# Kernel optimization log

Hardware: AMD Instinct MI355X
Metric: run time of the kernel (lower is better)

Reference implementation:

```python
import jax, jax.numpy as jnp
import numpy as np

D_MODEL = 1024
NUM_HEADS = 16
D_K = D_MODEL // NUM_HEADS
SCALE = float(np.sqrt(D_K))


def setup_inputs() -> dict:
    key = jax.random.key(0)
    ks = jax.random.split(key, 11)
    B, S = 4, 2048
    std = 1.0 / np.sqrt(D_MODEL)
    return {
        "query": jax.random.normal(ks[0], (B, S, D_MODEL), jnp.float32),
        "key": jax.random.normal(ks[1], (B, S, D_MODEL), jnp.float32),
        "value": jax.random.normal(ks[2], (B, S, D_MODEL), jnp.float32),
        "w_q": jax.random.normal(ks[3], (D_MODEL, D_MODEL), jnp.float32) * std,
        "b_q": jnp.zeros((D_MODEL,), jnp.float32),
        "w_k": jax.random.normal(ks[4], (D_MODEL, D_MODEL), jnp.float32) * std,
        "b_k": jnp.zeros((D_MODEL,), jnp.float32),
        "w_v": jax.random.normal(ks[5], (D_MODEL, D_MODEL), jnp.float32) * std,
        "b_v": jnp.zeros((D_MODEL,), jnp.float32),
        "w_o": jax.random.normal(ks[6], (D_MODEL, D_MODEL), jnp.float32) * std,
        "b_o": jnp.zeros((D_MODEL,), jnp.float32),
    }


def reference(query, key, value, w_q, b_q, w_k, b_k, w_v, b_v, w_o, b_o):
    B, S, _ = query.shape
    # torch Linear: x @ W.T + b
    def proj(x, w, b):
        y = x @ w.T + b                      # [B,S,D]
        return y.reshape(B, -1, NUM_HEADS, D_K).transpose(0, 2, 1, 3)  # [B,H,S,dk]

    Q = proj(query, w_q, b_q)
    K = proj(key, w_k, b_k)
    V = proj(value, w_v, b_v)

    scores = jnp.einsum("bhqd,bhkd->bhqk", Q, K) / SCALE   # [B,H,S,S]
    attn = jax.nn.softmax(scores, axis=-1)                  # dropout = identity (eval)
    ctx = jnp.einsum("bhqk,bhkd->bhqd", attn, V)            # [B,H,S,dk]
    ctx = ctx.transpose(0, 2, 1, 3).reshape(B, -1, D_MODEL) # [B,S,D]
    out = ctx @ w_o.T + b_o
    return out, attn
```

## Files before the change

kernel.cpp:

```cpp
#include <hip/hip_runtime.h>

typedef __bf16 bf16;
typedef __bf16 bf16x8 __attribute__((ext_vector_type(8)));
typedef __bf16 bf16x4 __attribute__((ext_vector_type(4)));
typedef float f32x4 __attribute__((ext_vector_type(4)));

#define B_SZ   4
#define S_LEN  2048
#define DM     1024
#define NH     16
#define DKH    64
#define MROWS  (B_SZ * S_LEN)

#if __has_builtin(__builtin_amdgcn_exp2f)
#define EXP2(x) __builtin_amdgcn_exp2f(x)
#else
#define EXP2(x) exp2f(x)
#endif

__device__ __forceinline__ int swz_(int row) { return ((row ^ (row >> 3)) & 7) << 4; }

__device__ __forceinline__ void gload_lds16(const void* g, void* l) {
  __builtin_amdgcn_global_load_lds(
      (const __attribute__((address_space(1))) void*)g,
      (__attribute__((address_space(3))) void*)l, 16, 0, 0);
}

__global__ __launch_bounds__(256) void cvt_f32_bf16(const float* __restrict__ in,
                                                    bf16* __restrict__ out, int n8) {
  for (int i = blockIdx.x * blockDim.x + threadIdx.x; i < n8; i += gridDim.x * blockDim.x) {
    const float4* p = (const float4*)(in + (size_t)i * 8);
    float4 a = p[0], b = p[1];
    bf16x8 o;
    o[0] = (bf16)a.x; o[1] = (bf16)a.y; o[2] = (bf16)a.z; o[3] = (bf16)a.w;
    o[4] = (bf16)b.x; o[5] = (bf16)b.y; o[6] = (bf16)b.z; o[7] = (bf16)b.w;
    *(bf16x8*)(out + (size_t)i * 8) = o;
  }
}

template <int MODE>
__global__ __launch_bounds__(256) void gemm_bt(const bf16* __restrict__ A,
                                               const bf16* __restrict__ Bm,
                                               const float* __restrict__ bias,
                                               void* __restrict__ out) {
  constexpr int BM = 128, BN = 128, BK = 64, K = DM, N = DM;
  __shared__ bf16 As[BM * BK];
  __shared__ bf16 Bs[BN * BK];
  const int tid = threadIdx.x;
  const int l = tid & 63;
  const int w = tid >> 6;
  const int wr = w >> 1, wc = w & 1;
  const int m0 = (blockIdx.x >> 3) * BM;
  const int n0 = (blockIdx.x & 7) * BN;
  const int lrow = l & 15;
  const int lk = (l >> 4) * 8;

  f32x4 acc[4][4] = {};

  for (int kt = 0; kt < K; kt += BK) {
    __syncthreads();
#pragma unroll
    for (int r = 0; r < 4; ++r) {
      int c = r * 256 + tid;
      int row = c >> 3;
      int cb = ((c & 7) * 16) ^ swz_(row);
      gload_lds16((const char*)(A + (size_t)(m0 + row) * K + kt) + cb, (char*)As + c * 16);
      gload_lds16((const char*)(Bm + (size_t)(n0 + row) * K + kt) + cb, (char*)Bs + c * 16);
    }
    __syncthreads();
#pragma unroll
    for (int kk = 0; kk < BK; kk += 32) {
      bf16x8 a[4], b[4];
#pragma unroll
      for (int i = 0; i < 4; ++i) {
        int ar = wr * 64 + i * 16 + lrow;
        int br = wc * 64 + i * 16 + lrow;
        a[i] = *(const bf16x8*)((const char*)As + ar * 128 + (((kk + lk) * 2) ^ swz_(ar)));
        b[i] = *(const bf16x8*)((const char*)Bs + br * 128 + (((kk + lk) * 2) ^ swz_(br)));
      }
#pragma unroll
      for (int i = 0; i < 4; ++i)
#pragma unroll
        for (int j = 0; j < 4; ++j)
          acc[i][j] = __builtin_amdgcn_mfma_f32_16x16x32_bf16(a[i], b[j], acc[i][j], 0, 0, 0);
    }
  }

#pragma unroll
  for (int i = 0; i < 4; ++i) {
#pragma unroll
    for (int j = 0; j < 4; ++j) {
#pragma unroll
      for (int r = 0; r < 4; ++r) {
        int row = m0 + wr * 64 + i * 16 + (l >> 4) * 4 + r;
        int col = n0 + wc * 64 + j * 16 + (l & 15);
        float v = acc[i][j][r] + bias[col];
        if (MODE == 0) {
          int bb = row >> 11, ss = row & 2047, hh = col >> 6, dd = col & 63;
          ((bf16*)out)[(((size_t)bb * NH + hh) * S_LEN + ss) * DKH + dd] = (bf16)v;
        } else {
          ((float*)out)[(size_t)row * N + col] = v;
        }
      }
    }
  }
}

__global__ __launch_bounds__(256, 3) void attn_fused(const bf16* __restrict__ Q,
                                                     const bf16* __restrict__ Kg,
                                                     const bf16* __restrict__ Vg,
                                                     float* __restrict__ attn,
                                                     bf16* __restrict__ ctx) {
  constexpr int QT = 128, KT = 64, PSP = 72, NT = S_LEN / KT;
  __shared__ bf16 Ks[KT * DKH];
  __shared__ bf16 Vts[DKH * KT];
  __shared__ bf16 Ps[QT * PSP];

  const int tid = threadIdx.x, l = tid & 63, w = tid >> 6;
  const int bh = blockIdx.x >> 4;
  const int q0 = (blockIdx.x & 15) * QT;
  const bf16* Qb = Q + (size_t)bh * S_LEN * DKH;
  const bf16* Kb = Kg + (size_t)bh * S_LEN * DKH;
  const bf16* Vb = Vg + (size_t)bh * S_LEN * DKH;
  const int lrow = l & 15, lk = (l >> 4) * 8;
  const int g4 = (l >> 4) * 4;
  const float c2 = 0.18033688011f;

  bf16x8 qf[2][2];
#pragma unroll
  for (int m = 0; m < 2; ++m)
#pragma unroll
    for (int h = 0; h < 2; ++h)
      qf[m][h] = *(const bf16x8*)(Qb + (size_t)(q0 + w * 32 + m * 16 + lrow) * DKH + h * 32 + lk);

  auto stageK = [&](int kt) {
#pragma unroll
    for (int r = 0; r < 2; ++r) {
      int c = r * 256 + tid;
      int row = c >> 3;
      int cb = ((c & 7) * 16) ^ swz_(row);
      gload_lds16((const char*)(Kb + (size_t)(kt + row) * DKH) + cb, (char*)Ks + c * 16);
    }
  };

  float lsum[2] = {0.f, 0.f};
  for (int t = 0; t < NT; ++t) {
    __syncthreads();
    stageK(t * KT);
    __syncthreads();
    f32x4 st[2][4] = {};
#pragma unroll
    for (int h = 0; h < 2; ++h)
#pragma unroll
      for (int n = 0; n < 4; ++n) {
        int kr = n * 16 + lrow;
        bf16x8 b = *(const bf16x8*)((const char*)Ks + kr * 128 + (((h * 32 + lk) * 2) ^ swz_(kr)));
        st[0][n] = __builtin_amdgcn_mfma_f32_16x16x32_bf16(b, qf[0][h], st[0][n], 0, 0, 0);
        st[1][n] = __builtin_amdgcn_mfma_f32_16x16x32_bf16(b, qf[1][h], st[1][n], 0, 0, 0);
      }
#pragma unroll
    for (int m = 0; m < 2; ++m)
#pragma unroll
      for (int n = 0; n < 4; ++n)
#pragma unroll
        for (int r = 0; r < 4; ++r)
          lsum[m] += EXP2(st[m][n][r] * c2);
  }

  float invl[2];
#pragma unroll
  for (int m = 0; m < 2; ++m) {
    float ll = lsum[m];
    ll += __shfl_xor(ll, 16);
    ll += __shfl_xor(ll, 32);
    invl[m] = 1.0f / ll;
  }

  f32x4 oc[2][4] = {};
  for (int t = 0; t < NT; ++t) {
    const int kt = t * KT;
    __syncthreads();
    stageK(kt);
    bf16x8 vv[2];
#pragma unroll
    for (int r = 0; r < 2; ++r) {
      int c = r * 256 + tid;
      vv[r] = *(const bf16x8*)(Vb + (size_t)(kt + (c >> 3)) * DKH + (c & 7) * 8);
    }
#pragma unroll
    for (int r = 0; r < 2; ++r) {
      int c = r * 256 + tid;
      int kv = c >> 3, d0 = (c & 7) * 8;
#pragma unroll
      for (int j = 0; j < 8; ++j) {
        int row = d0 + j;
        *(bf16*)((char*)Vts + row * 128 + ((kv * 2) ^ swz_(row))) = vv[r][j];
      }
    }
    __syncthreads();
    f32x4 st[2][4] = {};
#pragma unroll
    for (int h = 0; h < 2; ++h)
#pragma unroll
      for (int n = 0; n < 4; ++n) {
        int kr = n * 16 + lrow;
        bf16x8 b = *(const bf16x8*)((const char*)Ks + kr * 128 + (((h * 32 + lk) * 2) ^ swz_(kr)));
        st[0][n] = __builtin_amdgcn_mfma_f32_16x16x32_bf16(b, qf[0][h], st[0][n], 0, 0, 0);
        st[1][n] = __builtin_amdgcn_mfma_f32_16x16x32_bf16(b, qf[1][h], st[1][n], 0, 0, 0);
      }
#pragma unroll
    for (int m = 0; m < 2; ++m) {
      const int qr = w * 32 + m * 16 + lrow;
      float* arow = attn + (size_t)bh * S_LEN * S_LEN + (size_t)(q0 + qr) * S_LEN + kt + g4;
#pragma unroll
      for (int n = 0; n < 4; ++n) {
        f32x4 p4;
#pragma unroll
        for (int r = 0; r < 4; ++r) p4[r] = EXP2(st[m][n][r] * c2) * invl[m];
        *(f32x4*)(arow + n * 16) = p4;
        bf16x4 pk;
#pragma unroll
        for (int r = 0; r < 4; ++r) pk[r] = (bf16)p4[r];
        *(bf16x4*)((char*)Ps + qr * (PSP * 2) + n * 32 + g4 * 2) = pk;
      }
    }
    __syncthreads();
#pragma unroll
    for (int kk = 0; kk < KT; kk += 32) {
      bf16x8 bfr[4];
#pragma unroll
      for (int n = 0; n < 4; ++n) {
        int vr = n * 16 + lrow;
        bfr[n] = *(const bf16x8*)((const char*)Vts + vr * 128 + (((kk + lk) * 2) ^ swz_(vr)));
      }
#pragma unroll
      for (int m = 0; m < 2; ++m) {
        bf16x8 pa = *(const bf16x8*)(Ps + (w * 32 + m * 16 + lrow) * PSP + kk + lk);
#pragma unroll
        for (int n = 0; n < 4; ++n)
          oc[m][n] = __builtin_amdgcn_mfma_f32_16x16x32_bf16(pa, bfr[n], oc[m][n], 0, 0, 0);
      }
    }
  }

  const int bb = bh >> 4, hh = bh & 15;
#pragma unroll
  for (int m = 0; m < 2; ++m)
#pragma unroll
    for (int n = 0; n < 4; ++n)
#pragma unroll
      for (int r = 0; r < 4; ++r) {
        int row = q0 + w * 32 + m * 16 + (l >> 4) * 4 + r;
        int col = hh * DKH + n * 16 + (l & 15);
        ctx[((size_t)bb * S_LEN + row) * DM + col] = (bf16)oc[m][n][r];
      }
}

extern "C" void kernel_launch(void* const* d_in, const int* in_sizes, int n_in,
                              void* d_out, int out_size, void* d_ws, size_t ws_size,
                              hipStream_t stream) {
  const float* query = (const float*)d_in[0];
  const float* key_i = (const float*)d_in[1];
  const float* value = (const float*)d_in[2];
  const float* w_q = (const float*)d_in[3];
  const float* b_q = (const float*)d_in[4];
  const float* w_k = (const float*)d_in[5];
  const float* b_k = (const float*)d_in[6];
  const float* w_v = (const float*)d_in[7];
  const float* b_v = (const float*)d_in[8];
  const float* w_o = (const float*)d_in[9];
  const float* b_o = (const float*)d_in[10];

  char* ws = (char*)d_ws;
  bf16* Xb = (bf16*)(ws);
  bf16* Wb = (bf16*)(ws + ((size_t)16 << 20));
  bf16* Qb = (bf16*)(ws + ((size_t)18 << 20));
  bf16* Kb = (bf16*)(ws + ((size_t)34 << 20));
  bf16* Vb = (bf16*)(ws + ((size_t)50 << 20));
  bf16* Cb = (bf16*)(ws + ((size_t)66 << 20));

  float* outp = (float*)d_out;
  float* attnp = outp + (size_t)B_SZ * S_LEN * DM;

  const int NX = MROWS * DM / 8;
  const int NW = DM * DM / 8;
  dim3 blk(256);

  cvt_f32_bf16<<<2048, blk, 0, stream>>>(query, Xb, NX);
  cvt_f32_bf16<<<512, blk, 0, stream>>>(w_q, Wb, NW);
  gemm_bt<0><<<512, blk, 0, stream>>>(Xb, Wb, b_q, Qb);
  cvt_f32_bf16<<<2048, blk, 0, stream>>>(key_i, Xb, NX);
  cvt_f32_bf16<<<512, blk, 0, stream>>>(w_k, Wb, NW);
  gemm_bt<0><<<512, blk, 0, stream>>>(Xb, Wb, b_k, Kb);
  cvt_f32_bf16<<<2048, blk, 0, stream>>>(value, Xb, NX);
  cvt_f32_bf16<<<512, blk, 0, stream>>>(w_v, Wb, NW);
  gemm_bt<0><<<512, blk, 0, stream>>>(Xb, Wb, b_v, Vb);

  attn_fused<<<B_SZ * NH * (S_LEN / 128), blk, 0, stream>>>(Qb, Kb, Vb, attnp, Cb);

  cvt_f32_bf16<<<512, blk, 0, stream>>>(w_o, Wb, NW);
  gemm_bt<1><<<512, blk, 0, stream>>>(Cb, Wb, b_o, (void*)outp);
}
```

Baseline: 561.0 us.

## Pre-transpose V in a separate kernel and stage it into LDS asynchronously

```diff
diff --git a/kernel.cpp b/kernel.cpp
--- a/kernel.cpp
+++ b/kernel.cpp
@@ -35,6 +35,39 @@
     o[0] = (bf16)a.x; o[1] = (bf16)a.y; o[2] = (bf16)a.z; o[3] = (bf16)a.w;
     o[4] = (bf16)b.x; o[5] = (bf16)b.y; o[6] = (bf16)b.z; o[7] = (bf16)b.w;
     *(bf16x8*)(out + (size_t)i * 8) = o;
+  }
+}
+
+__global__ __launch_bounds__(256) void transpose_v(const bf16* __restrict__ V,
+                                                   bf16* __restrict__ VT) {
+  __shared__ bf16 T[64 * 64];
+  const int tid = threadIdx.x;
+  const int bh = blockIdx.x >> 5;
+  const int s0 = (blockIdx.x & 31) * 64;
+  const bf16* src = V + ((size_t)bh * S_LEN + s0) * DKH;
+  bf16x8 vv[2];
+#pragma unroll
+  for (int r = 0; r < 2; ++r) {
+    int c = r * 256 + tid;
+    vv[r] = *(const bf16x8*)(src + (c >> 3) * DKH + (c & 7) * 8);
+  }
+#pragma unroll
+  for (int r = 0; r < 2; ++r) {
+    int c = r * 256 + tid;
+    int s = c >> 3, d0 = (c & 7) * 8;
+#pragma unroll
+    for (int j = 0; j < 8; ++j) {
+      int row = d0 + j;
+      *(bf16*)((char*)T + row * 128 + ((s * 2) ^ swz_(row))) = vv[r][j];
+    }
+  }
+  __syncthreads();
+#pragma unroll
+  for (int r = 0; r < 2; ++r) {
+    int c = r * 256 + tid;
+    int d = c >> 3, off = (c & 7) * 16;
+    bf16x8 o = *(const bf16x8*)((const char*)T + d * 128 + (off ^ swz_(d)));
+    *(bf16x8*)(VT + ((size_t)bh * DKH + d) * S_LEN + s0 + (c & 7) * 8) = o;
   }
 }
 
@@ -108,7 +141,7 @@
 
 __global__ __launch_bounds__(256, 3) void attn_fused(const bf16* __restrict__ Q,
                                                      const bf16* __restrict__ Kg,
-                                                     const bf16* __restrict__ Vg,
+                                                     const bf16* __restrict__ VT,
                                                      float* __restrict__ attn,
                                                      bf16* __restrict__ ctx) {
   constexpr int QT = 128, KT = 64, PSP = 72, NT = S_LEN / KT;
@@ -121,7 +154,7 @@
   const int q0 = (blockIdx.x & 15) * QT;
   const bf16* Qb = Q + (size_t)bh * S_LEN * DKH;
   const bf16* Kb = Kg + (size_t)bh * S_LEN * DKH;
-  const bf16* Vb = Vg + (size_t)bh * S_LEN * DKH;
+  const bf16* VTb = VT + (size_t)bh * DKH * S_LEN;
   const int lrow = l & 15, lk = (l >> 4) * 8;
   const int g4 = (l >> 4) * 4;
   const float c2 = 0.18033688011f;
@@ -142,6 +175,15 @@
       gload_lds16((const char*)(Kb + (size_t)(kt + row) * DKH) + cb, (char*)Ks + c * 16);
     }
   };
+  auto stageV = [&](int kt) {
+#pragma unroll
+    for (int r = 0; r < 2; ++r) {
+      int c = r * 256 + tid;
+      int row = c >> 3;
+      int cb = ((c & 7) * 16) ^ swz_(row);
+      gload_lds16((const char*)(VTb + (size_t)row * S_LEN + kt) + cb, (char*)Vts + c * 16);
+    }
+  };
 
   float lsum[2] = {0.f, 0.f};
   for (int t = 0; t < NT; ++t) {
@@ -181,22 +223,7 @@
     const int kt = t * KT;
     __syncthreads();
     stageK(kt);
-    bf16x8 vv[2];
-#pragma unroll
-    for (int r = 0; r < 2; ++r) {
-      int c = r * 256 + tid;
-      vv[r] = *(const bf16x8*)(Vb + (size_t)(kt + (c >> 3)) * DKH + (c & 7) * 8);
-    }
-#pragma unroll
-    for (int r = 0; r < 2; ++r) {
-      int c = r * 256 + tid;
-      int kv = c >> 3, d0 = (c & 7) * 8;
-#pragma unroll
-      for (int j = 0; j < 8; ++j) {
-        int row = d0 + j;
-        *(bf16*)((char*)Vts + row * 128 + ((kv * 2) ^ swz_(row))) = vv[r][j];
-      }
-    }
+    stageV(kt);
     __syncthreads();
     f32x4 st[2][4] = {};
 #pragma unroll
@@ -224,7 +251,6 @@
         *(bf16x4*)((char*)Ps + qr * (PSP * 2) + n * 32 + g4 * 2) = pk;
       }
     }
-    __syncthreads();
 #pragma unroll
     for (int kk = 0; kk < KT; kk += 32) {
       bf16x8 bfr[4];
@@ -296,8 +322,10 @@
   cvt_f32_bf16<<<512, blk, 0, stream>>>(w_v, Wb, NW);
   gemm_bt<0><<<512, blk, 0, stream>>>(Xb, Wb, b_v, Vb);
 
-  attn_fused<<<B_SZ * NH * (S_LEN / 128), blk, 0, stream>>>(Qb, Kb, Vb, attnp, Cb);
-
+  transpose_v<<<B_SZ * NH * (S_LEN / 64), blk, 0, stream>>>(Vb, Xb);
   cvt_f32_bf16<<<512, blk, 0, stream>>>(w_o, Wb, NW);
+
+  attn_fused<<<B_SZ * NH * (S_LEN / 128), blk, 0, stream>>>(Qb, Kb, Xb, attnp, Cb);
+
   gemm_bt<1><<<512, blk, 0, stream>>>(Cb, Wb, b_o, (void*)outp);
 }
```

Result: faster. 549.5 us (-2.0%).
